# Optimization experiments

Hardware: AMD Instinct MI355X
Metric: run time of the kernel (lower is better)

## Reference

```python
import jax, jax.numpy as jnp
import numpy as np

N, IN_F, E, EDGE_F, H, C = 50000, 128, 800000, 32, 4, 32
NEG_SLOPE = 0.2
EPS = 1e-16


def setup_inputs() -> dict:
    key = jax.random.key(0)
    ks = jax.random.split(key, 10)
    s = lambda *sh: 1.0 / np.sqrt(sh[-1])
    return {
        "node_features": jax.random.normal(ks[0], (N, IN_F), jnp.float32),
        "edge_features": jax.random.normal(ks[1], (E, EDGE_F), jnp.float32),
        "edge_index": jax.random.randint(ks[2], (2, E), 0, N, jnp.int32),
        # GATConv params
        "W_gat": jax.random.normal(ks[3], (H * C, IN_F), jnp.float32) * s(IN_F),
        "att_src": jax.random.normal(ks[4], (H, C), jnp.float32) * s(C),
        "att_dst": jax.random.normal(ks[5], (H, C), jnp.float32) * s(C),
        "att_edge": jax.random.normal(ks[6], (H, C), jnp.float32) * s(C),
        "bias": jnp.zeros((H * C,), jnp.float32),
        # edge_linear and skip_connection weights
        "W_edge": jax.random.normal(ks[7], (H * C, EDGE_F), jnp.float32) * s(EDGE_F),
        "W_skip": jax.random.normal(ks[8], (H * C, IN_F), jnp.float32) * s(IN_F),
    }


def reference(node_features, edge_features, edge_index, W_gat, att_src, att_dst,
              att_edge, bias, W_edge, W_skip):
    src, dst = edge_index[0], edge_index[1]
    # edge_linear + view(-1, H, C)
    e_attr = (edge_features @ W_edge.T).reshape(E, H, C)
    # GATConv: per-head linear transform of nodes -> [N, H, C]
    x = (node_features @ W_gat.T).reshape(N, H, C)
    # attention logits: a_src.x_i + a_dst.x_j + a_edge.e  -> [E, H]
    a_src = jnp.einsum('nhc,hc->nh', x, att_src)
    a_dst = jnp.einsum('nhc,hc->nh', x, att_dst)
    a_edge = jnp.einsum('ehc,hc->eh', e_attr, att_edge)
    alpha = jax.nn.leaky_relu(a_src[src] + a_dst[dst] + a_edge, NEG_SLOPE)
    # segment softmax over incoming edges of each destination node
    m = jax.ops.segment_max(alpha, dst, num_segments=N)  # [N, H]
    m = jnp.where(jnp.isfinite(m), m, 0.0)
    ex = jnp.exp(alpha - m[dst])
    denom = jax.ops.segment_sum(ex, dst, num_segments=N)  # [N, H]
    attn = ex / (denom[dst] + EPS)  # [E, H]
    # message = alpha * x_src ; scatter-add to destination
    msg = x[src] * attn[:, :, None]  # [E, H, C]
    out = jax.ops.segment_sum(msg, dst, num_segments=N)  # [N, H, C]
    out = out.reshape(N, H * C) + bias  # concat=True
    # skip connection + ELU activation
    out = out + node_features @ W_skip.T
    return jax.nn.elu(out)
```

## Files before the change

kernel.cpp:

```cpp
#include <hip/hip_runtime.h>
#include <hip/hip_bf16.h>

constexpr int N_NODES = 50000;
constexpr int IN_F    = 128;
constexpr long E_EDGES = 800000;
constexpr int EDGE_F  = 32;
constexpr int H_HEADS = 4;
constexpr int C_CH    = 32;
constexpr int HC      = 128;
constexpr float NEG_SLOPE = 0.2f;
constexpr float EPS = 1e-16f;
constexpr int B_HIST = 64;
constexpr int B_WCAT = 8;
constexpr int CHUNK  = (int)(E_EDGES / B_HIST);
constexpr int HWORDS = N_NODES / 2;
constexpr int NB_SCAN = (N_NODES + 255) / 256;
constexpr int NB_EL4  = (int)((E_EDGES + 1023) / 1024);
constexpr int NB_AE10 = (int)((E_EDGES + 511) / 512);
constexpr float SM_SHIFT = 12.0f;

typedef __attribute__((ext_vector_type(8))) short bf16x8;
typedef __attribute__((ext_vector_type(4))) float f32x4;

__device__ __forceinline__ unsigned short f2b(float f) {
    __hip_bfloat16 h = __float2bfloat16(f);
    return *reinterpret_cast<unsigned short*>(&h);
}
__device__ __forceinline__ float b2f_lo(unsigned v) { return __uint_as_float(v << 16); }
__device__ __forceinline__ float b2f_hi(unsigned v) { return __uint_as_float(v & 0xffff0000u); }

__global__ __launch_bounds__(1024) void mega1_kernel(
    const int* __restrict__ dst, unsigned int* __restrict__ histB,
    unsigned short* __restrict__ rank16, const float* __restrict__ ef,
    const float* __restrict__ We, const float* __restrict__ att_edge,
    const float* __restrict__ Wg, const float* __restrict__ Ws,
    unsigned short* __restrict__ wcat, float* __restrict__ ae)
{
    __shared__ unsigned int h[HWORDS];
    __shared__ float wf_lds[128];
    const int b = blockIdx.x, t = threadIdx.x;

    if (b < B_HIST) {
        for (int i = t; i < HWORDS; i += 1024) h[i] = 0;
        __syncthreads();
        const int e0 = b * CHUNK;
        for (int i = t; i < CHUNK; i += 1024) {
            int d = dst[e0 + i];
            int sh = (d & 1) * 16;
            unsigned old = atomicAdd(&h[d >> 1], 1u << sh);
            rank16[e0 + i] = (unsigned short)((old >> sh) & 0xFFFFu);
        }
        __syncthreads();
        unsigned int* outp = histB + (size_t)b * HWORDS;
        for (int i = t; i < HWORDS; i += 1024) outp[i] = h[i];
        return;
    }

    if (b < B_HIST + B_WCAT) {
        int i = ((b - B_HIST) * 1024 + t) * 4;
        const float* srcp = (i < 16384) ? (Wg + i) : (Ws + i - 16384);
        float4 v = *(const float4*)srcp;
        ushort4 o;
        o.x = f2b(v.x); o.y = f2b(v.y); o.z = f2b(v.z); o.w = f2b(v.w);
        *(ushort4*)&wcat[i] = o;
        return;
    }

    if (t < 128) {
        int hh = t >> 5, f = t & 31;
        float acc = 0.f;
#pragma unroll
        for (int c = 0; c < C_CH; ++c)
            acc = fmaf(We[(hh * C_CH + c) * EDGE_F + f], att_edge[hh * C_CH + c], acc);
        wf_lds[t] = acc;
    }
    __syncthreads();

    const int l = t & 63, wv = t >> 6;
    const int sub = l & 3, eIdx = l >> 2;
    const long eb = (long)(b - B_HIST - B_WCAT) * 512 + wv * 32 + eIdx;
    const float4* ef4 = (const float4*)ef;
    float4 wa[4], wb[4];
#pragma unroll
    for (int hh = 0; hh < 4; ++hh) {
        wa[hh] = *(const float4*)&wf_lds[hh * 32 + sub * 4];
        wb[hh] = *(const float4*)&wf_lds[hh * 32 + 16 + sub * 4];
    }

    if (eb < E_EDGES) {
        float4 a0 = ef4[eb * 8 + sub];
        float4 b0 = ef4[eb * 8 + 4 + sub];
        float p[4];
#pragma unroll
        for (int hh = 0; hh < 4; ++hh) {
            float acc = 0.f;
            acc = fmaf(a0.x, wa[hh].x, acc); acc = fmaf(a0.y, wa[hh].y, acc);
            acc = fmaf(a0.z, wa[hh].z, acc); acc = fmaf(a0.w, wa[hh].w, acc);
            acc = fmaf(b0.x, wb[hh].x, acc); acc = fmaf(b0.y, wb[hh].y, acc);
            acc = fmaf(b0.z, wb[hh].z, acc); acc = fmaf(b0.w, wb[hh].w, acc);
            p[hh] = acc;
        }
#pragma unroll
        for (int hh = 0; hh < 4; ++hh) {
            p[hh] += __shfl_xor(p[hh], 1);
            p[hh] += __shfl_xor(p[hh], 2);
        }
        float v0 = (sub == 0) ? p[0] : (sub == 1) ? p[1] : (sub == 2) ? p[2] : p[3];
        ae[eb * 4 + sub] = v0;
    }
    if (eb + 16 < E_EDGES) {
        float4 a1 = ef4[(eb + 16) * 8 + sub];
        float4 b1 = ef4[(eb + 16) * 8 + 4 + sub];
        float p[4];
#pragma unroll
        for (int hh = 0; hh < 4; ++hh) {
            float acc = 0.f;
            acc = fmaf(a1.x, wa[hh].x, acc); acc = fmaf(a1.y, wa[hh].y, acc);
            acc = fmaf(a1.z, wa[hh].z, acc); acc = fmaf(a1.w, wa[hh].w, acc);
            acc = fmaf(b1.x, wb[hh].x, acc); acc = fmaf(b1.y, wb[hh].y, acc);
            acc = fmaf(b1.z, wb[hh].z, acc); acc = fmaf(b1.w, wb[hh].w, acc);
            p[hh] = acc;
        }
#pragma unroll
        for (int hh = 0; hh < 4; ++hh) {
            p[hh] += __shfl_xor(p[hh], 1);
            p[hh] += __shfl_xor(p[hh], 2);
        }
        float v1 = (sub == 0) ? p[0] : (sub == 1) ? p[1] : (sub == 2) ? p[2] : p[3];
        ae[(eb + 16) * 4 + sub] = v1;
    }
}

__global__ __launch_bounds__(256) void mfma_gemm_kernel(
    const float* __restrict__ nf, const unsigned short* __restrict__ wcat,
    const float* __restrict__ bias, unsigned short* __restrict__ xb,
    float* __restrict__ out)
{
    const int t  = threadIdx.x;
    const int w  = t >> 6;
    const int l  = t & 63;
    const int lr = l & 15;
    const int lk = l >> 4;
    const int n0 = blockIdx.x * 64;

    bf16x8 bfr[4][4];
#pragma unroll
    for (int nfr = 0; nfr < 4; ++nfr)
#pragma unroll
        for (int ks = 0; ks < 4; ++ks)
            bfr[nfr][ks] = *(const bf16x8*)&wcat[(w * 64 + nfr * 16 + lr) * 128 + ks * 32 + lk * 8];

    f32x4 acc[4][4];
#pragma unroll
    for (int mf = 0; mf < 4; ++mf)
#pragma unroll
        for (int nfr = 0; nfr < 4; ++nfr)
            acc[mf][nfr] = (f32x4){0.f, 0.f, 0.f, 0.f};

#pragma unroll
    for (int ks = 0; ks < 4; ++ks) {
        bf16x8 afr[4];
#pragma unroll
        for (int mf = 0; mf < 4; ++mf) {
            int row = n0 + mf * 16 + lr;
            row = row < N_NODES ? row : N_NODES - 1;
            const float* ap = nf + (size_t)row * IN_F + ks * 32 + lk * 8;
            float4 a0 = *(const float4*)ap;
            float4 a1 = *(const float4*)(ap + 4);
            bf16x8 f;
            f[0] = (short)f2b(a0.x); f[1] = (short)f2b(a0.y);
            f[2] = (short)f2b(a0.z); f[3] = (short)f2b(a0.w);
            f[4] = (short)f2b(a1.x); f[5] = (short)f2b(a1.y);
            f[6] = (short)f2b(a1.z); f[7] = (short)f2b(a1.w);
            afr[mf] = f;
        }
#pragma unroll
        for (int mf = 0; mf < 4; ++mf)
#pragma unroll
            for (int nfr = 0; nfr < 4; ++nfr)
                acc[mf][nfr] = __builtin_amdgcn_mfma_f32_16x16x32_bf16(
                    afr[mf], bfr[nfr][ks], acc[mf][nfr], 0, 0, 0);
    }

#pragma unroll
    for (int nfr = 0; nfr < 4; ++nfr) {
        const int gc = w * 64 + nfr * 16 + lr;
        if (gc < HC) {
#pragma unroll
            for (int mf = 0; mf < 4; ++mf)
#pragma unroll
                for (int r = 0; r < 4; ++r) {
                    int m = n0 + mf * 16 + lk * 4 + r;
                    if (m < N_NODES) xb[(size_t)m * HC + gc] = f2b(acc[mf][nfr][r]);
                }
        } else {
            const float bv = bias[gc - HC];
#pragma unroll
            for (int mf = 0; mf < 4; ++mf)
#pragma unroll
                for (int r = 0; r < 4; ++r) {
                    int m = n0 + mf * 16 + lk * 4 + r;
                    if (m < N_NODES) out[(size_t)m * HC + gc - HC] = acc[mf][nfr][r] + bv;
                }
        }
    }
}

__global__ __launch_bounds__(256) void a_kernel(
    const unsigned int* __restrict__ xb32, const float* __restrict__ att_src,
    const float* __restrict__ att_dst, float* __restrict__ asrc,
    float* __restrict__ adst)
{
    const int wave = threadIdx.x >> 6, lane = threadIdx.x & 63;
    const int n = blockIdx.x * 4 + wave;
    if (n >= N_NODES) return;
    unsigned v = xb32[(size_t)n * 64 + lane];
    float x0 = b2f_lo(v), x1 = b2f_hi(v);
    float2 as = ((const float2*)att_src)[lane];
    float2 ad = ((const float2*)att_dst)[lane];
    float ps = x0 * as.x + x1 * as.y;
    float pd = x0 * ad.x + x1 * ad.y;
#pragma unroll
    for (int off = 1; off < 16; off <<= 1) {
        ps += __shfl_xor(ps, off);
        pd += __shfl_xor(pd, off);
    }
    if ((lane & 15) == 0) {
        asrc[(size_t)n * H_HEADS + (lane >> 4)] = ps;
        adst[(size_t)n * H_HEADS + (lane >> 4)] = pd;
    }
}

__global__ __launch_bounds__(256) void scan1_kernel(const unsigned int* __restrict__ histB,
                                                    int* __restrict__ row_ptr,
                                                    int* __restrict__ blocksum)
{
    __shared__ int s[256];
    int t = threadIdx.x;
    int i = blockIdx.x * 256 + t;
    int v = 0;
    if (i < N_NODES) {
        int w = i >> 1, sh = (i & 1) * 16;
#pragma unroll 8
        for (int b = 0; b < B_HIST; ++b)
            v += (int)((histB[(size_t)b * HWORDS + w] >> sh) & 0xFFFFu);
    }
    s[t] = v;
    __syncthreads();
#pragma unroll
    for (int off = 1; off < 256; off <<= 1) {
        int u = (t >= off) ? s[t - off] : 0;
        __syncthreads();
        s[t] += u;
        __syncthreads();
    }
    if (i < N_NODES) row_ptr[i] = s[t] - v;
    if (t == 255) blocksum[blockIdx.x] = s[255];
}

__global__ __launch_bounds__(256) void scanF_kernel(int* __restrict__ row_ptr,
                                                    const int* __restrict__ blocksum,
                                                    const unsigned int* __restrict__ histB,
                                                    int* __restrict__ off)
{
    __shared__ int s[256];
    int t = threadIdx.x;
    int v = (t < NB_SCAN) ? blocksum[t] : 0;
    s[t] = v;
    __syncthreads();
#pragma unroll
    for (int o = 1; o < 256; o <<= 1) {
        int u = (t >= o) ? s[t - o] : 0;
        __syncthreads();
        s[t] += u;
        __syncthreads();
    }
    int excl = s[t] - v;
    __syncthreads();
    s[t] = excl;
    __syncthreads();
    const int blockoff = s[blockIdx.x];

    int i = blockIdx.x * 256 + t;
    if (i < N_NODES) {
        int run = row_ptr[i] + blockoff;
        row_ptr[i] = run;
        int w = i >> 1, sh = (i & 1) * 16;
#pragma unroll 8
        for (int b = 0; b < B_HIST; ++b) {
            off[(size_t)b * N_NODES + i] = run;
            run += (int)((histB[(size_t)b * HWORDS + w] >> sh) & 0xFFFFu);
        }
    }
    if (i == 0) row_ptr[N_NODES] = (int)E_EDGES;
}

__global__ __launch_bounds__(256) void edge_logits_kernel(
    const int* __restrict__ src, const int* __restrict__ dst,
    const float* __restrict__ ae, const float* __restrict__ asrc,
    const float* __restrict__ adst, const int* __restrict__ off,
    const unsigned short* __restrict__ rank16, uint4* __restrict__ rec4)
{
    const long base = (long)blockIdx.x * 1024 + threadIdx.x;

    int s[4], d[4], rk[4];
    float4 a_e[4];
    bool val[4];
    long ec[4];
#pragma unroll
    for (int j = 0; j < 4; ++j) {
        long e = base + j * 256;
        val[j] = e < E_EDGES;
        ec[j] = val[j] ? e : 0;
        s[j]  = src[ec[j]];
        d[j]  = dst[ec[j]];
        rk[j] = (int)rank16[ec[j]];
        a_e[j] = ((const float4*)ae)[ec[j]];
    }
    float4 as4[4], ad4[4];
    int pos[4];
#pragma unroll
    for (int j = 0; j < 4; ++j) {
        as4[j] = ((const float4*)asrc)[s[j]];
        ad4[j] = ((const float4*)adst)[d[j]];
        int be = (int)(ec[j] / CHUNK);
        pos[j] = off[(size_t)be * N_NODES + d[j]] + rk[j];
    }
#pragma unroll
    for (int j = 0; j < 4; ++j) {
        if (!val[j]) continue;
        float lg[4] = {as4[j].x + ad4[j].x + a_e[j].x, as4[j].y + ad4[j].y + a_e[j].y,
                       as4[j].z + ad4[j].z + a_e[j].z, as4[j].w + ad4[j].w + a_e[j].w};
        uint4 r;
        unsigned* rw = (unsigned*)&r;
#pragma unroll
        for (int h = 0; h < 4; ++h) {
            float al = lg[h] > 0.f ? lg[h] : NEG_SLOPE * lg[h];
            rw[h] = (__float_as_uint(al) & 0xFFFFFF00u)
                  | ((unsigned)(s[j] >> (8 * h)) & 0xFFu);
        }
        rec4[pos[j]] = r;
    }
}

__device__ __forceinline__ void accum8(float* acc, uint4 v, float e) {
    acc[0] = fmaf(b2f_lo(v.x), e, acc[0]);
    acc[1] = fmaf(b2f_hi(v.x), e, acc[1]);
    acc[2] = fmaf(b2f_lo(v.y), e, acc[2]);
    acc[3] = fmaf(b2f_hi(v.y), e, acc[3]);
    acc[4] = fmaf(b2f_lo(v.z), e, acc[4]);
    acc[5] = fmaf(b2f_hi(v.z), e, acc[5]);
    acc[6] = fmaf(b2f_lo(v.w), e, acc[6]);
    acc[7] = fmaf(b2f_hi(v.w), e, acc[7]);
}

__device__ __forceinline__ int rec_src(uint4 r) {
    return (int)((r.x & 0xFFu) | ((r.y & 0xFFu) << 8));
}
__device__ __forceinline__ float rec_alpha(uint4 r, int h) {
    unsigned w = h == 0 ? r.x : h == 1 ? r.y : h == 2 ? r.z : r.w;
    return __uint_as_float(w & 0xFFFFFF00u);
}

__global__ __launch_bounds__(256) void aggregate_kernel(
    const int* __restrict__ row_ptr, const uint4* __restrict__ rec4,
    const uint4* __restrict__ xb4, float* __restrict__ out)
{
    const int wave = threadIdx.x >> 6;
    const int lane = threadIdx.x & 63;
    const int d = blockIdx.x * 4 + wave;
    if (d >= N_NODES) return;
    const int beg = row_ptr[d], end = row_ptr[d + 1];
    const int q  = lane >> 4;
    const int cg = lane & 15;
    const int h  = cg >> 2;

    float acc[8] = {0.f, 0.f, 0.f, 0.f, 0.f, 0.f, 0.f, 0.f};
    float dsum = 0.f;

    int i = beg;
    for (; i + 8 <= end; i += 8) {
        int i0 = i + q, i1 = i + 4 + q;
        uint4 r0 = rec4[i0];
        uint4 r1 = rec4[i1];
        int s0 = rec_src(r0);
        int s1 = rec_src(r1);
        float a0 = rec_alpha(r0, h);
        float a1 = rec_alpha(r1, h);
        uint4 v0 = xb4[(size_t)s0 * 16 + cg];
        uint4 v1 = xb4[(size_t)s1 * 16 + cg];
        float e0 = __expf(a0 - SM_SHIFT);
        float e1 = __expf(a1 - SM_SHIFT);
        dsum += e0 + e1;
        accum8(acc, v0, e0);
        accum8(acc, v1, e1);
    }
    for (; i < end; i += 4) {
        int idx = i + q;
        bool val = idx < end;
        int ii = val ? idx : end - 1;
        uint4 r = rec4[ii];
        int s = rec_src(r);
        float a = rec_alpha(r, h);
        uint4 v = xb4[(size_t)s * 16 + cg];
        float e = val ? __expf(a - SM_SHIFT) : 0.f;
        dsum += e;
        accum8(acc, v, e);
    }

#pragma unroll
    for (int off = 16; off <= 32; off <<= 1) {
        dsum += __shfl_xor(dsum, off);
#pragma unroll
        for (int k = 0; k < 8; ++k) acc[k] += __shfl_xor(acc[k], off);
    }
    const float inv = 1.f / (dsum + EPS);

    if (q == 0) {
        float* op = out + (size_t)d * HC + cg * 8;
        float4 o0 = *(const float4*)op;
        float4 o1 = *(const float4*)(op + 4);
        o0.x += acc[0] * inv; o0.y += acc[1] * inv;
        o0.z += acc[2] * inv; o0.w += acc[3] * inv;
        o1.x += acc[4] * inv; o1.y += acc[5] * inv;
        o1.z += acc[6] * inv; o1.w += acc[7] * inv;
        o0.x = o0.x > 0.f ? o0.x : expf(o0.x) - 1.f;
        o0.y = o0.y > 0.f ? o0.y : expf(o0.y) - 1.f;
        o0.z = o0.z > 0.f ? o0.z : expf(o0.z) - 1.f;
        o0.w = o0.w > 0.f ? o0.w : expf(o0.w) - 1.f;
        o1.x = o1.x > 0.f ? o1.x : expf(o1.x) - 1.f;
        o1.y = o1.y > 0.f ? o1.y : expf(o1.y) - 1.f;
        o1.z = o1.z > 0.f ? o1.z : expf(o1.z) - 1.f;
        o1.w = o1.w > 0.f ? o1.w : expf(o1.w) - 1.f;
        *(float4*)op = o0;
        *(float4*)(op + 4) = o1;
    }
}

extern "C" void kernel_launch(void* const* d_in, const int* in_sizes, int n_in,
                              void* d_out, int out_size, void* d_ws, size_t ws_size,
                              hipStream_t stream)
{
    const float* nf       = (const float*)d_in[0];
    const float* ef       = (const float*)d_in[1];
    const int*   ei       = (const int*)d_in[2];
    const float* Wg       = (const float*)d_in[3];
    const float* att_src  = (const float*)d_in[4];
    const float* att_dst  = (const float*)d_in[5];
    const float* att_edge = (const float*)d_in[6];
    const float* bias     = (const float*)d_in[7];
    const float* We       = (const float*)d_in[8];
    const float* Ws       = (const float*)d_in[9];
    float* out = (float*)d_out;

    const int* src = ei;
    const int* dst = ei + E_EDGES;

    unsigned int* rec   = (unsigned int*)d_ws;
    float* ae           = (float*)(rec + 4 * E_EDGES);
    unsigned short* xb  = (unsigned short*)(ae + 4 * E_EDGES);
    unsigned short* wcat= xb + (size_t)N_NODES * HC;
    float* asrc         = (float*)(wcat + 256 * 128);
    float* adst         = asrc + (size_t)N_NODES * H_HEADS;
    unsigned int* histB = (unsigned int*)(adst + (size_t)N_NODES * H_HEADS);
    int*   off          = (int*)(histB + (size_t)B_HIST * HWORDS);
    int*   row_ptr      = off + (size_t)B_HIST * N_NODES;
    int*   blocksum     = row_ptr + N_NODES + 1;
    unsigned short* rank16 = (unsigned short*)(blocksum + 256);

    mega1_kernel<<<B_HIST + B_WCAT + NB_AE10, 1024, 0, stream>>>(
        dst, histB, rank16, ef, We, att_edge, Wg, Ws, wcat, ae);
    mfma_gemm_kernel<<<(N_NODES + 63) / 64, 256, 0, stream>>>(
        nf, wcat, bias, xb, out);
    a_kernel<<<(N_NODES + 3) / 4, 256, 0, stream>>>(
        (const unsigned int*)xb, att_src, att_dst, asrc, adst);
    scan1_kernel<<<NB_SCAN, 256, 0, stream>>>(histB, row_ptr, blocksum);
    scanF_kernel<<<NB_SCAN, 256, 0, stream>>>(row_ptr, blocksum, histB, off);
    edge_logits_kernel<<<NB_EL4, 256, 0, stream>>>(
        src, dst, ae, asrc, adst, off, rank16, (uint4*)rec);
    aggregate_kernel<<<(N_NODES + 3) / 4, 256, 0, stream>>>(
        row_ptr, (const uint4*)rec, (const uint4*)xb, out);
}
```

Measured before the change: 160.7 us.

## Move attention logit assembly into aggregation and fuse scan with node-score kernel

```diff
diff --git a/kernel.cpp b/kernel.cpp
--- a/kernel.cpp
+++ b/kernel.cpp
@@ -10,11 +10,12 @@
 constexpr int HC      = 128;
 constexpr float NEG_SLOPE = 0.2f;
 constexpr float EPS = 1e-16f;
-constexpr int B_HIST = 64;
+constexpr int B_HIST = 128;
 constexpr int B_WCAT = 8;
 constexpr int CHUNK  = (int)(E_EDGES / B_HIST);
 constexpr int HWORDS = N_NODES / 2;
 constexpr int NB_SCAN = (N_NODES + 255) / 256;
+constexpr int NB_A    = (N_NODES + 3) / 4;
 constexpr int NB_EL4  = (int)((E_EDGES + 1023) / 1024);
 constexpr int NB_AE10 = (int)((E_EDGES + 511) / 512);
 constexpr float SM_SHIFT = 12.0f;
@@ -206,13 +207,39 @@
     }
 }
 
-__global__ __launch_bounds__(256) void a_kernel(
-    const unsigned int* __restrict__ xb32, const float* __restrict__ att_src,
-    const float* __restrict__ att_dst, float* __restrict__ asrc,
-    float* __restrict__ adst)
-{
-    const int wave = threadIdx.x >> 6, lane = threadIdx.x & 63;
-    const int n = blockIdx.x * 4 + wave;
+__global__ __launch_bounds__(256) void scan1_a_kernel(
+    const unsigned int* __restrict__ histB, int* __restrict__ row_ptr,
+    int* __restrict__ blocksum, const unsigned int* __restrict__ xb32,
+    const float* __restrict__ att_src, const float* __restrict__ att_dst,
+    float* __restrict__ asrc, float* __restrict__ adst)
+{
+    const int b = blockIdx.x, t = threadIdx.x;
+    if (b < NB_SCAN) {
+        __shared__ int s[256];
+        int i = b * 256 + t;
+        int v = 0;
+        if (i < N_NODES) {
+            int w = i >> 1, sh = (i & 1) * 16;
+#pragma unroll 8
+            for (int bb = 0; bb < B_HIST; ++bb)
+                v += (int)((histB[(size_t)bb * HWORDS + w] >> sh) & 0xFFFFu);
+        }
+        s[t] = v;
+        __syncthreads();
+#pragma unroll
+        for (int off = 1; off < 256; off <<= 1) {
+            int u = (t >= off) ? s[t - off] : 0;
+            __syncthreads();
+            s[t] += u;
+            __syncthreads();
+        }
+        if (i < N_NODES) row_ptr[i] = s[t] - v;
+        if (t == 255) blocksum[b] = s[255];
+        return;
+    }
+
+    const int wave = t >> 6, lane = t & 63;
+    const int n = (b - NB_SCAN) * 4 + wave;
     if (n >= N_NODES) return;
     unsigned v = xb32[(size_t)n * 64 + lane];
     float x0 = b2f_lo(v), x1 = b2f_hi(v);
@@ -229,33 +256,6 @@
         asrc[(size_t)n * H_HEADS + (lane >> 4)] = ps;
         adst[(size_t)n * H_HEADS + (lane >> 4)] = pd;
     }
-}
-
-__global__ __launch_bounds__(256) void scan1_kernel(const unsigned int* __restrict__ histB,
-                                                    int* __restrict__ row_ptr,
-                                                    int* __restrict__ blocksum)
-{
-    __shared__ int s[256];
-    int t = threadIdx.x;
-    int i = blockIdx.x * 256 + t;
-    int v = 0;
-    if (i < N_NODES) {
-        int w = i >> 1, sh = (i & 1) * 16;
-#pragma unroll 8
-        for (int b = 0; b < B_HIST; ++b)
-            v += (int)((histB[(size_t)b * HWORDS + w] >> sh) & 0xFFFFu);
-    }
-    s[t] = v;
-    __syncthreads();
-#pragma unroll
-    for (int off = 1; off < 256; off <<= 1) {
-        int u = (t >= off) ? s[t - off] : 0;
-        __syncthreads();
-        s[t] += u;
-        __syncthreads();
-    }
-    if (i < N_NODES) row_ptr[i] = s[t] - v;
-    if (t == 255) blocksum[blockIdx.x] = s[255];
 }
 
 __global__ __launch_bounds__(256) void scanF_kernel(int* __restrict__ row_ptr,
@@ -297,8 +297,7 @@
 
 __global__ __launch_bounds__(256) void edge_logits_kernel(
     const int* __restrict__ src, const int* __restrict__ dst,
-    const float* __restrict__ ae, const float* __restrict__ asrc,
-    const float* __restrict__ adst, const int* __restrict__ off,
+    const float* __restrict__ ae, const int* __restrict__ off,
     const unsigned short* __restrict__ rank16, uint4* __restrict__ rec4)
 {
     const long base = (long)blockIdx.x * 1024 + threadIdx.x;
@@ -317,26 +316,21 @@
         rk[j] = (int)rank16[ec[j]];
         a_e[j] = ((const float4*)ae)[ec[j]];
     }
-    float4 as4[4], ad4[4];
     int pos[4];
 #pragma unroll
     for (int j = 0; j < 4; ++j) {
-        as4[j] = ((const float4*)asrc)[s[j]];
-        ad4[j] = ((const float4*)adst)[d[j]];
         int be = (int)(ec[j] / CHUNK);
         pos[j] = off[(size_t)be * N_NODES + d[j]] + rk[j];
     }
 #pragma unroll
     for (int j = 0; j < 4; ++j) {
         if (!val[j]) continue;
-        float lg[4] = {as4[j].x + ad4[j].x + a_e[j].x, as4[j].y + ad4[j].y + a_e[j].y,
-                       as4[j].z + ad4[j].z + a_e[j].z, as4[j].w + ad4[j].w + a_e[j].w};
         uint4 r;
         unsigned* rw = (unsigned*)&r;
+        const float* av = (const float*)&a_e[j];
 #pragma unroll
         for (int h = 0; h < 4; ++h) {
-            float al = lg[h] > 0.f ? lg[h] : NEG_SLOPE * lg[h];
-            rw[h] = (__float_as_uint(al) & 0xFFFFFF00u)
+            rw[h] = (__float_as_uint(av[h]) & 0xFFFFFF00u)
                   | ((unsigned)(s[j] >> (8 * h)) & 0xFFu);
         }
         rec4[pos[j]] = r;
@@ -357,14 +351,15 @@
 __device__ __forceinline__ int rec_src(uint4 r) {
     return (int)((r.x & 0xFFu) | ((r.y & 0xFFu) << 8));
 }
-__device__ __forceinline__ float rec_alpha(uint4 r, int h) {
+__device__ __forceinline__ float rec_ae(uint4 r, int h) {
     unsigned w = h == 0 ? r.x : h == 1 ? r.y : h == 2 ? r.z : r.w;
     return __uint_as_float(w & 0xFFFFFF00u);
 }
 
 __global__ __launch_bounds__(256) void aggregate_kernel(
     const int* __restrict__ row_ptr, const uint4* __restrict__ rec4,
-    const uint4* __restrict__ xb4, float* __restrict__ out)
+    const uint4* __restrict__ xb4, const float* __restrict__ asrc,
+    const float* __restrict__ adst, float* __restrict__ out)
 {
     const int wave = threadIdx.x >> 6;
     const int lane = threadIdx.x & 63;
@@ -375,6 +370,8 @@
     const int cg = lane & 15;
     const int h  = cg >> 2;
 
+    const float adv = adst[(size_t)d * 4 + h];
+
     float acc[8] = {0.f, 0.f, 0.f, 0.f, 0.f, 0.f, 0.f, 0.f};
     float dsum = 0.f;
 
@@ -385,12 +382,18 @@
         uint4 r1 = rec4[i1];
         int s0 = rec_src(r0);
         int s1 = rec_src(r1);
-        float a0 = rec_alpha(r0, h);
-        float a1 = rec_alpha(r1, h);
+        float g0 = rec_ae(r0, h);
+        float g1 = rec_ae(r1, h);
+        float as0 = asrc[(size_t)s0 * 4 + h];
+        float as1 = asrc[(size_t)s1 * 4 + h];
         uint4 v0 = xb4[(size_t)s0 * 16 + cg];
         uint4 v1 = xb4[(size_t)s1 * 16 + cg];
-        float e0 = __expf(a0 - SM_SHIFT);
-        float e1 = __expf(a1 - SM_SHIFT);
+        float lg0 = as0 + adv + g0;
+        float lg1 = as1 + adv + g1;
+        float al0 = lg0 > 0.f ? lg0 : NEG_SLOPE * lg0;
+        float al1 = lg1 > 0.f ? lg1 : NEG_SLOPE * lg1;
+        float e0 = __expf(al0 - SM_SHIFT);
+        float e1 = __expf(al1 - SM_SHIFT);
         dsum += e0 + e1;
         accum8(acc, v0, e0);
         accum8(acc, v1, e1);
@@ -401,9 +404,12 @@
         int ii = val ? idx : end - 1;
         uint4 r = rec4[ii];
         int s = rec_src(r);
-        float a = rec_alpha(r, h);
+        float g = rec_ae(r, h);
+        float as0 = asrc[(size_t)s * 4 + h];
         uint4 v = xb4[(size_t)s * 16 + cg];
-        float e = val ? __expf(a - SM_SHIFT) : 0.f;
+        float lg = as0 + adv + g;
+        float al = lg > 0.f ? lg : NEG_SLOPE * lg;
+        float e = val ? __expf(al - SM_SHIFT) : 0.f;
         dsum += e;
         accum8(acc, v, e);
     }
@@ -472,12 +478,12 @@
         dst, histB, rank16, ef, We, att_edge, Wg, Ws, wcat, ae);
     mfma_gemm_kernel<<<(N_NODES + 63) / 64, 256, 0, stream>>>(
         nf, wcat, bias, xb, out);
-    a_kernel<<<(N_NODES + 3) / 4, 256, 0, stream>>>(
-        (const unsigned int*)xb, att_src, att_dst, asrc, adst);
-    scan1_kernel<<<NB_SCAN, 256, 0, stream>>>(histB, row_ptr, blocksum);
+    scan1_a_kernel<<<NB_SCAN + NB_A, 256, 0, stream>>>(
+        histB, row_ptr, blocksum, (const unsigned int*)xb,
+        att_src, att_dst, asrc, adst);
     scanF_kernel<<<NB_SCAN, 256, 0, stream>>>(row_ptr, blocksum, histB, off);
     edge_logits_kernel<<<NB_EL4, 256, 0, stream>>>(
-        src, dst, ae, asrc, adst, off, rank16, (uint4*)rec);
+        src, dst, ae, off, rank16, (uint4*)rec);
     aggregate_kernel<<<(N_NODES + 3) / 4, 256, 0, stream>>>(
-        row_ptr, (const uint4*)rec, (const uint4*)xb, out);
-}
+        row_ptr, (const uint4*)rec, (const uint4*)xb, asrc, adst, out);
+}
```

Measured after the change: 161.7 us. About the same (+0.6%).

## Pack histogram counts into 8-bit fields and fuse scan1 with attention-dot kernel

Applied to the files above, without the earlier changes.

```diff
diff --git a/kernel.cpp b/kernel.cpp
--- a/kernel.cpp
+++ b/kernel.cpp
@@ -13,8 +13,9 @@
 constexpr int B_HIST = 64;
 constexpr int B_WCAT = 8;
 constexpr int CHUNK  = (int)(E_EDGES / B_HIST);
-constexpr int HWORDS = N_NODES / 2;
+constexpr int HW8    = N_NODES / 4;
 constexpr int NB_SCAN = (N_NODES + 255) / 256;
+constexpr int NB_A    = (N_NODES + 3) / 4;
 constexpr int NB_EL4  = (int)((E_EDGES + 1023) / 1024);
 constexpr int NB_AE10 = (int)((E_EDGES + 511) / 512);
 constexpr float SM_SHIFT = 12.0f;
@@ -36,23 +37,23 @@
     const float* __restrict__ Wg, const float* __restrict__ Ws,
     unsigned short* __restrict__ wcat, float* __restrict__ ae)
 {
-    __shared__ unsigned int h[HWORDS];
+    __shared__ unsigned int h[HW8];
     __shared__ float wf_lds[128];
     const int b = blockIdx.x, t = threadIdx.x;
 
     if (b < B_HIST) {
-        for (int i = t; i < HWORDS; i += 1024) h[i] = 0;
+        for (int i = t; i < HW8; i += 1024) h[i] = 0;
         __syncthreads();
         const int e0 = b * CHUNK;
         for (int i = t; i < CHUNK; i += 1024) {
             int d = dst[e0 + i];
-            int sh = (d & 1) * 16;
-            unsigned old = atomicAdd(&h[d >> 1], 1u << sh);
-            rank16[e0 + i] = (unsigned short)((old >> sh) & 0xFFFFu);
+            int sh = (d & 3) * 8;
+            unsigned old = atomicAdd(&h[d >> 2], 1u << sh);
+            rank16[e0 + i] = (unsigned short)((old >> sh) & 0xFFu);
         }
         __syncthreads();
-        unsigned int* outp = histB + (size_t)b * HWORDS;
-        for (int i = t; i < HWORDS; i += 1024) outp[i] = h[i];
+        unsigned int* outp = histB + (size_t)b * HW8;
+        for (int i = t; i < HW8; i += 1024) outp[i] = h[i];
         return;
     }
 
@@ -206,13 +207,39 @@
     }
 }
 
-__global__ __launch_bounds__(256) void a_kernel(
-    const unsigned int* __restrict__ xb32, const float* __restrict__ att_src,
-    const float* __restrict__ att_dst, float* __restrict__ asrc,
-    float* __restrict__ adst)
-{
-    const int wave = threadIdx.x >> 6, lane = threadIdx.x & 63;
-    const int n = blockIdx.x * 4 + wave;
+__global__ __launch_bounds__(256) void scan1_a_kernel(
+    const unsigned int* __restrict__ histB, int* __restrict__ row_ptr,
+    int* __restrict__ blocksum, const unsigned int* __restrict__ xb32,
+    const float* __restrict__ att_src, const float* __restrict__ att_dst,
+    float* __restrict__ asrc, float* __restrict__ adst)
+{
+    const int b = blockIdx.x, t = threadIdx.x;
+    if (b < NB_SCAN) {
+        __shared__ int s[256];
+        int i = b * 256 + t;
+        int v = 0;
+        if (i < N_NODES) {
+            int w = i >> 2, sh = (i & 3) * 8;
+#pragma unroll 8
+            for (int bb = 0; bb < B_HIST; ++bb)
+                v += (int)((histB[(size_t)bb * HW8 + w] >> sh) & 0xFFu);
+        }
+        s[t] = v;
+        __syncthreads();
+#pragma unroll
+        for (int off = 1; off < 256; off <<= 1) {
+            int u = (t >= off) ? s[t - off] : 0;
+            __syncthreads();
+            s[t] += u;
+            __syncthreads();
+        }
+        if (i < N_NODES) row_ptr[i] = s[t] - v;
+        if (t == 255) blocksum[b] = s[255];
+        return;
+    }
+
+    const int wave = t >> 6, lane = t & 63;
+    const int n = (b - NB_SCAN) * 4 + wave;
     if (n >= N_NODES) return;
     unsigned v = xb32[(size_t)n * 64 + lane];
     float x0 = b2f_lo(v), x1 = b2f_hi(v);
@@ -231,33 +258,6 @@
     }
 }
 
-__global__ __launch_bounds__(256) void scan1_kernel(const unsigned int* __restrict__ histB,
-                                                    int* __restrict__ row_ptr,
-                                                    int* __restrict__ blocksum)
-{
-    __shared__ int s[256];
-    int t = threadIdx.x;
-    int i = blockIdx.x * 256 + t;
-    int v = 0;
-    if (i < N_NODES) {
-        int w = i >> 1, sh = (i & 1) * 16;
-#pragma unroll 8
-        for (int b = 0; b < B_HIST; ++b)
-            v += (int)((histB[(size_t)b * HWORDS + w] >> sh) & 0xFFFFu);
-    }
-    s[t] = v;
-    __syncthreads();
-#pragma unroll
-    for (int off = 1; off < 256; off <<= 1) {
-        int u = (t >= off) ? s[t - off] : 0;
-        __syncthreads();
-        s[t] += u;
-        __syncthreads();
-    }
-    if (i < N_NODES) row_ptr[i] = s[t] - v;
-    if (t == 255) blocksum[blockIdx.x] = s[255];
-}
-
 __global__ __launch_bounds__(256) void scanF_kernel(int* __restrict__ row_ptr,
                                                     const int* __restrict__ blocksum,
                                                     const unsigned int* __restrict__ histB,
@@ -285,11 +285,11 @@
     if (i < N_NODES) {
         int run = row_ptr[i] + blockoff;
         row_ptr[i] = run;
-        int w = i >> 1, sh = (i & 1) * 16;
+        int w = i >> 2, sh = (i & 3) * 8;
 #pragma unroll 8
         for (int b = 0; b < B_HIST; ++b) {
             off[(size_t)b * N_NODES + i] = run;
-            run += (int)((histB[(size_t)b * HWORDS + w] >> sh) & 0xFFFFu);
+            run += (int)((histB[(size_t)b * HW8 + w] >> sh) & 0xFFu);
         }
     }
     if (i == 0) row_ptr[N_NODES] = (int)E_EDGES;
@@ -463,7 +463,7 @@
     float* asrc         = (float*)(wcat + 256 * 128);
     float* adst         = asrc + (size_t)N_NODES * H_HEADS;
     unsigned int* histB = (unsigned int*)(adst + (size_t)N_NODES * H_HEADS);
-    int*   off          = (int*)(histB + (size_t)B_HIST * HWORDS);
+    int*   off          = (int*)(histB + (size_t)B_HIST * HW8);
     int*   row_ptr      = off + (size_t)B_HIST * N_NODES;
     int*   blocksum     = row_ptr + N_NODES + 1;
     unsigned short* rank16 = (unsigned short*)(blocksum + 256);
@@ -472,9 +472,9 @@
         dst, histB, rank16, ef, We, att_edge, Wg, Ws, wcat, ae);
     mfma_gemm_kernel<<<(N_NODES + 63) / 64, 256, 0, stream>>>(
         nf, wcat, bias, xb, out);
-    a_kernel<<<(N_NODES + 3) / 4, 256, 0, stream>>>(
-        (const unsigned int*)xb, att_src, att_dst, asrc, adst);
-    scan1_kernel<<<NB_SCAN, 256, 0, stream>>>(histB, row_ptr, blocksum);
+    scan1_a_kernel<<<NB_SCAN + NB_A, 256, 0, stream>>>(
+        histB, row_ptr, blocksum, (const unsigned int*)xb,
+        att_src, att_dst, asrc, adst);
     scanF_kernel<<<NB_SCAN, 256, 0, stream>>>(row_ptr, blocksum, histB, off);
     edge_logits_kernel<<<NB_EL4, 256, 0, stream>>>(
         src, dst, ae, asrc, adst, off, rank16, (uint4*)rec);
```

New measurement: 155.6 us. 1.03x faster.
